# Optimization experiments

Measured on AMD Instinct MI355X. Metric: run time of the kernel, lower is better.

## Reference

```python
import jax, jax.numpy as jnp
import numpy as np

N_NODES = 100000
N_EDGES = 640000
NODE_DIM = 128
EDGE_DIM = 64
NUM_HEADS = 4
EPS = 1e-6


def setup_inputs() -> dict:
    key = jax.random.key(0)
    ks = jax.random.split(key, 12)
    s_attn = 1.0 / np.sqrt(NODE_DIM + EDGE_DIM)
    s_ev = 1.0 / np.sqrt(EDGE_DIM)
    s_out = 1.0 / np.sqrt(NODE_DIM)
    return {
        "node_features": jax.random.normal(ks[0], (N_NODES, NODE_DIM), jnp.float32),
        "edge_features": jax.random.normal(ks[1], (N_EDGES, EDGE_DIM), jnp.float32),
        "attn_W": jax.random.uniform(ks[2], (NODE_DIM + EDGE_DIM, NUM_HEADS), jnp.float32, -s_attn, s_attn),
        "attn_b": jax.random.uniform(ks[3], (NUM_HEADS,), jnp.float32, -s_attn, s_attn),
        "ev_W": jax.random.uniform(ks[4], (EDGE_DIM, NODE_DIM), jnp.float32, -s_ev, s_ev),
        "ev_b": jax.random.uniform(ks[5], (NODE_DIM,), jnp.float32, -s_ev, s_ev),
        "out1_W": jax.random.uniform(ks[6], (NODE_DIM, NODE_DIM), jnp.float32, -s_out, s_out),
        "out1_b": jax.random.uniform(ks[7], (NODE_DIM,), jnp.float32, -s_out, s_out),
        "out2_W": jax.random.uniform(ks[8], (NODE_DIM, NODE_DIM), jnp.float32, -s_out, s_out),
        "out2_b": jax.random.uniform(ks[9], (NODE_DIM,), jnp.float32, -s_out, s_out),
        "edge_index": jax.random.randint(ks[10], (2, N_EDGES), 0, N_NODES, jnp.int64 if jax.config.jax_enable_x64 else jnp.int32),
    }


def _segment_softmax_aggregate(values, scores_mean, dst, num_nodes):
    # segment max (empty segments -> -inf, then zeroed, matching torch include_self=False path)
    max_scores = jax.ops.segment_max(scores_mean, dst, num_segments=num_nodes)
    max_scores = jnp.where(jnp.isneginf(max_scores), jnp.zeros_like(max_scores), max_scores)
    exp_scores = jnp.exp(scores_mean - max_scores[dst])            # (E,)
    sum_exp = jax.ops.segment_sum(exp_scores, dst, num_segments=num_nodes)
    attn_weights = exp_scores / (sum_exp[dst] + EPS)               # (E,)
    # weighted scatter-add of edge values into destination nodes
    return jax.ops.segment_sum(values * attn_weights[:, None], dst, num_segments=num_nodes)


def reference(node_features, edge_features, attn_W, attn_b, ev_W, ev_b,
              out1_W, out1_b, out2_W, out2_b, edge_index):
    num_nodes = node_features.shape[0]
    dst = edge_index[1]
    h_dst = node_features[dst]                                     # (E, node_dim) gather
    attn_input = jnp.concatenate([h_dst, edge_features], axis=1)   # (E, node_dim+edge_dim)
    attn_scores = attn_input @ attn_W + attn_b                     # (E, H)
    scores_mean = attn_scores.mean(axis=1)                         # (E,)
    edge_values = edge_features @ ev_W + ev_b                      # (E, node_dim)
    messages = _segment_softmax_aggregate(edge_values, scores_mean, dst, num_nodes)
    update = jax.nn.relu(messages @ out1_W + out1_b) @ out2_W + out2_b
    return node_features + update
```

## Files before the change

### kernel.cpp

```cpp
#include <hip/hip_runtime.h>
#include <cstddef>

#define NN 100000
#define NE 640000
#define NB_SCAN 391
#define NTILE 1563

typedef short  short8   __attribute__((ext_vector_type(8)));
typedef float  f32x4    __attribute__((ext_vector_type(4)));
typedef ushort ushort4v __attribute__((ext_vector_type(4)));

__device__ __forceinline__ short f2bf(float f) {
    union { float f; unsigned u; } v; v.f = f;
    unsigned r = (v.u + 0x7fffu + ((v.u >> 16) & 1u)) >> 16;
    return (short)r;
}

__global__ __launch_bounds__(256) void k_pre(
    const float* __restrict__ W2, const int* __restrict__ dst_idx,
    int* __restrict__ count, ushort* __restrict__ W2t)
{
    const int gid = blockIdx.x * 256 + threadIdx.x;
    if (gid < 16384) {
        const int n = gid >> 7, k = gid & 127;
        W2t[gid] = (ushort)f2bf(W2[k * 128 + n]);
    }
    atomicAdd(&count[dst_idx[gid]], 1);
}

__global__ __launch_bounds__(128) void k_wfuse(
    const float* __restrict__ evW, const float* __restrict__ evb,
    const float* __restrict__ W1,
    ushort* __restrict__ EVW1t, float* __restrict__ EVB1)
{
    const int j = blockIdx.x;
    const int n = threadIdx.x;
    float acc = 0.f;
    #pragma unroll 8
    for (int c = 0; c < 128; ++c)
        acc = fmaf(evW[j * 128 + c], W1[c * 128 + n], acc);
    EVW1t[n * 64 + j] = (ushort)f2bf(acc);
    if (j == 0) {
        float ab = 0.f;
        #pragma unroll 8
        for (int c = 0; c < 128; ++c)
            ab = fmaf(evb[c], W1[c * 128 + n], ab);
        EVB1[n] = ab;
    }
}

__global__ __launch_bounds__(256) void k_scan_bsum(
    const int* __restrict__ count, int* __restrict__ bsum)
{
    __shared__ int s[256];
    const int t = threadIdx.x, i = blockIdx.x * 256 + t;
    s[t] = (i < NN) ? count[i] : 0;
    __syncthreads();
    for (int off = 128; off; off >>= 1) { if (t < off) s[t] += s[t + off]; __syncthreads(); }
    if (t == 0) bsum[blockIdx.x] = s[0];
}

__global__ __launch_bounds__(256) void k_scan_final(
    const int* __restrict__ count, const int* __restrict__ bsum,
    int* __restrict__ rowptr)
{
    __shared__ int s[256];
    __shared__ int red[4];
    const int t = threadIdx.x, i = blockIdx.x * 256 + t;
    const int v = (i < NN) ? count[i] : 0;
    s[t] = v;

    int part = 0;
    for (int b = t; b < blockIdx.x; b += 256) part += bsum[b];
    #pragma unroll
    for (int off = 32; off; off >>= 1) part += __shfl_xor(part, off);
    if ((t & 63) == 0) red[t >> 6] = part;
    __syncthreads();
    const int boff = red[0] + red[1] + red[2] + red[3];

    for (int off = 1; off < 256; off <<= 1) {
        const int x = (t >= off) ? s[t - off] : 0;
        __syncthreads();
        s[t] += x;
        __syncthreads();
    }
    if (i < NN) rowptr[i] = boff + s[t] - v;
    if (blockIdx.x == NB_SCAN - 1 && t == 255) rowptr[NN] = boff + s[255];
}

__global__ __launch_bounds__(256) void k_permute(
    const int* __restrict__ dst_idx, const int* __restrict__ rowptr,
    int* cursor, int* __restrict__ perm)
{
    const int e = blockIdx.x * 256 + threadIdx.x;
    const int dd = dst_idx[e];
    perm[rowptr[dd] + atomicAdd(&cursor[dd], 1)] = e;
}

__global__ __launch_bounds__(256) void k_agg_gather(
    const float* __restrict__ ef, const float* __restrict__ attn_W,
    const int* __restrict__ perm, const int* __restrict__ rowptr,
    ushort* __restrict__ agg, float* __restrict__ msum)
{
    const int t  = threadIdx.x;
    const int sl = t & 15;
    const int n  = blockIdx.x * 16 + (t >> 4);
    const int beg = rowptr[n], end = rowptr[n + 1];

    float4 wl;
    {
        const float4 r0 = *reinterpret_cast<const float4*>(attn_W + (128 + sl * 4 + 0) * 4);
        const float4 r1 = *reinterpret_cast<const float4*>(attn_W + (128 + sl * 4 + 1) * 4);
        const float4 r2 = *reinterpret_cast<const float4*>(attn_W + (128 + sl * 4 + 2) * 4);
        const float4 r3 = *reinterpret_cast<const float4*>(attn_W + (128 + sl * 4 + 3) * 4);
        wl.x = 0.25f * (r0.x + r0.y + r0.z + r0.w);
        wl.y = 0.25f * (r1.x + r1.y + r1.z + r1.w);
        wl.z = 0.25f * (r2.x + r2.y + r2.z + r2.w);
        wl.w = 0.25f * (r3.x + r3.y + r3.z + r3.w);
    }

    float m  = -3.0e38f;
    float se = 0.f;
    f32x4 acc = {0.f, 0.f, 0.f, 0.f};

    for (int i = beg; i < end; i += 8) {
        int pe[8];
        #pragma unroll
        for (int j = 0; j < 8; ++j)
            pe[j] = perm[(i + j < end) ? (i + j) : beg];
        float4 v[8];
        #pragma unroll
        for (int j = 0; j < 8; ++j)
            v[j] = *reinterpret_cast<const float4*>(ef + (size_t)pe[j] * 64 + sl * 4);
        float sc[8];
        #pragma unroll
        for (int j = 0; j < 8; ++j) {
            float x = v[j].x * wl.x + v[j].y * wl.y + v[j].z * wl.z + v[j].w * wl.w;
            #pragma unroll
            for (int off = 8; off; off >>= 1) x += __shfl_xor(x, off, 16);
            sc[j] = (i + j < end) ? x : -3.0e38f;
        }
        float bm = m;
        #pragma unroll
        for (int j = 0; j < 8; ++j) bm = fmaxf(bm, sc[j]);
        const float r = __expf(m - bm);
        acc[0] *= r; acc[1] *= r; acc[2] *= r; acc[3] *= r; se *= r;
        m = bm;
        #pragma unroll
        for (int j = 0; j < 8; ++j) {
            const float w = __expf(sc[j] - m);
            acc[0] = fmaf(w, v[j].x, acc[0]);
            acc[1] = fmaf(w, v[j].y, acc[1]);
            acc[2] = fmaf(w, v[j].z, acc[2]);
            acc[3] = fmaf(w, v[j].w, acc[3]);
            se += w;
        }
    }

    ushort4v o;
    o[0] = (ushort)f2bf(acc[0]); o[1] = (ushort)f2bf(acc[1]);
    o[2] = (ushort)f2bf(acc[2]); o[3] = (ushort)f2bf(acc[3]);
    *reinterpret_cast<ushort4v*>(agg + (size_t)n * 64 + sl * 4) = o;
    if (sl == 0) msum[n] = se;
}

__global__ __launch_bounds__(256, 3) void k_mega(
    const ushort* __restrict__ agg, const float* __restrict__ msum,
    const ushort* __restrict__ EVW1t, const float* __restrict__ EVB1,
    const float* __restrict__ b1, const ushort* __restrict__ W2t,
    const float* __restrict__ b2, const float* __restrict__ nf,
    ushort* __restrict__ h1w, float* __restrict__ out)
{
    __shared__ ushort wlds[128 * 128];
    __shared__ ushort tl[4][16][136];

    const int tid  = threadIdx.x;
    const int wid  = tid >> 6;
    const int lane = tid & 63;
    const int r    = lane & 15;
    const int g    = lane >> 4;
    const int prow = lane >> 2;
    const int pc   = lane & 3;

    for (int c = tid; c < 1024; c += 256) {
        const int n = c >> 3, k8 = c & 7;
        *reinterpret_cast<short8*>(&wlds[n * 64 + ((k8 ^ (n & 7)) * 8)]) =
            *reinterpret_cast<const short8*>(EVW1t + n * 64 + k8 * 8);
    }
    __syncthreads();

    float evb1c[8], b1c[8];
    #pragma unroll
    for (int nt = 0; nt < 8; ++nt) {
        evb1c[nt] = EVB1[nt * 16 + r];
        b1c[nt]   = b1[nt * 16 + r];
    }

    for (int bt = blockIdx.x; bt < NTILE; bt += gridDim.x) {
        const int n0 = bt * 64 + wid * 16;
        if (n0 >= NN) continue;
        const short8 aev0 = *reinterpret_cast<const short8*>(agg + (size_t)(n0 + r) * 64 + g * 8);
        const short8 aev1 = *reinterpret_cast<const short8*>(agg + (size_t)(n0 + r) * 64 + 32 + g * 8);
        float cf[4], cb[4];
        #pragma unroll
        for (int i = 0; i < 4; ++i) {
            const float s = msum[n0 + g * 4 + i];
            const float c = 1.f / (s + 1e-6f);
            cf[i] = c; cb[i] = s * c;
        }
        #pragma unroll
        for (int nt = 0; nt < 8; ++nt) {
            const int row = nt * 16 + r;
            const short8 w0 = *reinterpret_cast<const short8*>(
                &wlds[row * 64 + (((0 + g) ^ (r & 7)) * 8)]);
            const short8 w1 = *reinterpret_cast<const short8*>(
                &wlds[row * 64 + (((4 + g) ^ (r & 7)) * 8)]);
            f32x4 acc = {0.f, 0.f, 0.f, 0.f};
            acc = __builtin_amdgcn_mfma_f32_16x16x32_bf16(aev0, w0, acc, 0, 0, 0);
            acc = __builtin_amdgcn_mfma_f32_16x16x32_bf16(aev1, w1, acc, 0, 0, 0);
            #pragma unroll
            for (int i = 0; i < 4; ++i) {
                const float h = fmaxf(cf[i] * acc[i] + cb[i] * evb1c[nt] + b1c[nt], 0.f);
                tl[wid][g * 4 + i][nt * 16 + r] = (ushort)f2bf(h);
            }
        }
        asm volatile("s_waitcnt lgkmcnt(0)" ::: "memory");
        ushort* hrow = h1w + (size_t)(n0 + prow) * 128 + pc * 8;
        #pragma unroll
        for (int ch = 0; ch < 4; ++ch)
            *reinterpret_cast<short8*>(hrow + ch * 32) =
                *reinterpret_cast<const short8*>(&tl[wid][prow][pc * 8 + ch * 32]);
    }

    __syncthreads();
    for (int c = tid; c < 2048; c += 256) {
        const int n = c >> 4, k8 = c & 15;
        *reinterpret_cast<short8*>(&wlds[n * 128 + ((k8 ^ (n & 7)) * 8)]) =
            *reinterpret_cast<const short8*>(W2t + n * 128 + k8 * 8);
    }
    __syncthreads();

    float b2c[8];
    #pragma unroll
    for (int nt = 0; nt < 8; ++nt) b2c[nt] = b2[nt * 16 + r];

    for (int bt = blockIdx.x; bt < NTILE; bt += gridDim.x) {
        const int n0 = bt * 64 + wid * 16;
        if (n0 >= NN) continue;
        short8 a2[4];
        #pragma unroll
        for (int t = 0; t < 4; ++t)
            a2[t] = *reinterpret_cast<const short8*>(
                h1w + (size_t)(n0 + r) * 128 + t * 32 + g * 8);
        #pragma unroll
        for (int nt = 0; nt < 8; ++nt) {
            f32x4 acc = {0.f, 0.f, 0.f, 0.f};
            #pragma unroll
            for (int t = 0; t < 4; ++t) {
                const short8 w = *reinterpret_cast<const short8*>(
                    &wlds[(nt * 16 + r) * 128 + (((t * 4 + g) ^ (r & 7)) * 8)]);
                acc = __builtin_amdgcn_mfma_f32_16x16x32_bf16(a2[t], w, acc, 0, 0, 0);
            }
            #pragma unroll
            for (int i = 0; i < 4; ++i) {
                const size_t idx = (size_t)(n0 + g * 4 + i) * 128 + nt * 16 + r;
                out[idx] = nf[idx] + acc[i] + b2c[nt];
            }
        }
    }
}

extern "C" void kernel_launch(void* const* d_in, const int* in_sizes, int n_in,
                              void* d_out, int out_size, void* d_ws, size_t ws_size,
                              hipStream_t stream)
{
    const float* nf     = (const float*)d_in[0];
    const float* ef     = (const float*)d_in[1];
    const float* attn_W = (const float*)d_in[2];
    const float* evW    = (const float*)d_in[4];
    const float* evb    = (const float*)d_in[5];
    const float* W1     = (const float*)d_in[6];
    const float* b1     = (const float*)d_in[7];
    const float* W2     = (const float*)d_in[8];
    const float* b2     = (const float*)d_in[9];
    const int*   eidx   = (const int*)d_in[10];
    const int*   dst    = eidx + NE;
    float* out = (float*)d_out;

    char* ws = (char*)d_ws;
    int*    count  = (int*)   (ws + 0);
    int*    cursor = (int*)   (ws + 400000);
    int*    rowptr = (int*)   (ws + 800000);
    float*  msum   = (float*) (ws + 1200128);
    int*    perm   = (int*)   (ws + 1600128);
    ushort* agg    = (ushort*)(ws + 4160128);
    ushort* W2t    = (ushort*)(ws + 16960128);
    ushort* EVW1t  = (ushort*)(ws + 16992896);
    float*  EVB1   = (float*) (ws + 17009280);
    int*    bsum   = (int*)   (ws + 17009792);
    ushort* h1w    = (ushort*)(ws + 17011456);

    hipMemsetAsync(count, 0, 800000, stream);

    k_pre        <<<2500, 256, 0, stream>>>(W2, dst, count, W2t);
    k_wfuse      <<<64,   128, 0, stream>>>(evW, evb, W1, EVW1t, EVB1);
    k_scan_bsum  <<<NB_SCAN, 256, 0, stream>>>(count, bsum);
    k_scan_final <<<NB_SCAN, 256, 0, stream>>>(count, bsum, rowptr);
    k_permute    <<<2500, 256, 0, stream>>>(dst, rowptr, cursor, perm);
    k_agg_gather <<<6250, 256, 0, stream>>>(ef, attn_W, perm, rowptr, agg, msum);
    k_mega       <<<768,  256, 0, stream>>>(agg, msum, EVW1t, EVB1, b1, W2t, b2,
                                            nf, h1w, out);
}
```

Baseline: 157.8 us.

## Fuse both MLP layers per tile via LDS and replace memset with zero kernel

The two MLP phases in k_mega previously went through a global bf16 h1 buffer with a grid-wide second pass. Now both weight matrices stay resident in LDS, and each wave feeds its hidden tile straight from LDS into the second GEMM, so the h1 global write and read-back disappear. The larger LDS footprint drops occupancy to 2 blocks per CU and the grid to 512 blocks. The hipMemsetAsync is also replaced by a small zeroing kernel, likely to cut per-call API overhead.

New measurement: 145.1 us. -8.0%, faster.

```diff
diff --git a/kernel.cpp b/kernel.cpp
--- a/kernel.cpp
+++ b/kernel.cpp
@@ -14,6 +14,11 @@
     union { float f; unsigned u; } v; v.f = f;
     unsigned r = (v.u + 0x7fffu + ((v.u >> 16) & 1u)) >> 16;
     return (short)r;
+}
+
+__global__ __launch_bounds__(256) void k_zero(int4* __restrict__ p) {
+    const int i = blockIdx.x * 256 + threadIdx.x;
+    if (i < 50000) p[i] = make_int4(0, 0, 0, 0);
 }
 
 __global__ __launch_bounds__(256) void k_pre(
@@ -164,14 +169,15 @@
     if (sl == 0) msum[n] = se;
 }
 
-__global__ __launch_bounds__(256, 3) void k_mega(
+__global__ __launch_bounds__(256, 2) void k_mega(
     const ushort* __restrict__ agg, const float* __restrict__ msum,
     const ushort* __restrict__ EVW1t, const float* __restrict__ EVB1,
     const float* __restrict__ b1, const ushort* __restrict__ W2t,
     const float* __restrict__ b2, const float* __restrict__ nf,
-    ushort* __restrict__ h1w, float* __restrict__ out)
-{
-    __shared__ ushort wlds[128 * 128];
+    float* __restrict__ out)
+{
+    __shared__ ushort wev[128 * 64];
+    __shared__ ushort ww2[128 * 128];
     __shared__ ushort tl[4][16][136];
 
     const int tid  = threadIdx.x;
@@ -179,26 +185,31 @@
     const int lane = tid & 63;
     const int r    = lane & 15;
     const int g    = lane >> 4;
-    const int prow = lane >> 2;
-    const int pc   = lane & 3;
 
     for (int c = tid; c < 1024; c += 256) {
         const int n = c >> 3, k8 = c & 7;
-        *reinterpret_cast<short8*>(&wlds[n * 64 + ((k8 ^ (n & 7)) * 8)]) =
+        *reinterpret_cast<short8*>(&wev[n * 64 + ((k8 ^ (n & 7)) * 8)]) =
             *reinterpret_cast<const short8*>(EVW1t + n * 64 + k8 * 8);
     }
+    for (int c = tid; c < 2048; c += 256) {
+        const int n = c >> 4, k8 = c & 15;
+        *reinterpret_cast<short8*>(&ww2[n * 128 + ((k8 ^ (n & 7)) * 8)]) =
+            *reinterpret_cast<const short8*>(W2t + n * 128 + k8 * 8);
+    }
     __syncthreads();
 
-    float evb1c[8], b1c[8];
+    float evb1c[8], b1c[8], b2c[8];
     #pragma unroll
     for (int nt = 0; nt < 8; ++nt) {
         evb1c[nt] = EVB1[nt * 16 + r];
         b1c[nt]   = b1[nt * 16 + r];
+        b2c[nt]   = b2[nt * 16 + r];
     }
 
     for (int bt = blockIdx.x; bt < NTILE; bt += gridDim.x) {
         const int n0 = bt * 64 + wid * 16;
         if (n0 >= NN) continue;
+
         const short8 aev0 = *reinterpret_cast<const short8*>(agg + (size_t)(n0 + r) * 64 + g * 8);
         const short8 aev1 = *reinterpret_cast<const short8*>(agg + (size_t)(n0 + r) * 64 + 32 + g * 8);
         float cf[4], cb[4];
@@ -208,13 +219,14 @@
             const float c = 1.f / (s + 1e-6f);
             cf[i] = c; cb[i] = s * c;
         }
+
         #pragma unroll
         for (int nt = 0; nt < 8; ++nt) {
             const int row = nt * 16 + r;
             const short8 w0 = *reinterpret_cast<const short8*>(
-                &wlds[row * 64 + (((0 + g) ^ (r & 7)) * 8)]);
+                &wev[row * 64 + (((0 + g) ^ (r & 7)) * 8)]);
             const short8 w1 = *reinterpret_cast<const short8*>(
-                &wlds[row * 64 + (((4 + g) ^ (r & 7)) * 8)]);
+                &wev[row * 64 + (((4 + g) ^ (r & 7)) * 8)]);
             f32x4 acc = {0.f, 0.f, 0.f, 0.f};
             acc = __builtin_amdgcn_mfma_f32_16x16x32_bf16(aev0, w0, acc, 0, 0, 0);
             acc = __builtin_amdgcn_mfma_f32_16x16x32_bf16(aev1, w1, acc, 0, 0, 0);
@@ -225,40 +237,20 @@
             }
         }
         asm volatile("s_waitcnt lgkmcnt(0)" ::: "memory");
-        ushort* hrow = h1w + (size_t)(n0 + prow) * 128 + pc * 8;
-        #pragma unroll
-        for (int ch = 0; ch < 4; ++ch)
-            *reinterpret_cast<short8*>(hrow + ch * 32) =
-                *reinterpret_cast<const short8*>(&tl[wid][prow][pc * 8 + ch * 32]);
-    }
-
-    __syncthreads();
-    for (int c = tid; c < 2048; c += 256) {
-        const int n = c >> 4, k8 = c & 15;
-        *reinterpret_cast<short8*>(&wlds[n * 128 + ((k8 ^ (n & 7)) * 8)]) =
-            *reinterpret_cast<const short8*>(W2t + n * 128 + k8 * 8);
-    }
-    __syncthreads();
-
-    float b2c[8];
-    #pragma unroll
-    for (int nt = 0; nt < 8; ++nt) b2c[nt] = b2[nt * 16 + r];
-
-    for (int bt = blockIdx.x; bt < NTILE; bt += gridDim.x) {
-        const int n0 = bt * 64 + wid * 16;
-        if (n0 >= NN) continue;
+
         short8 a2[4];
         #pragma unroll
         for (int t = 0; t < 4; ++t)
-            a2[t] = *reinterpret_cast<const short8*>(
-                h1w + (size_t)(n0 + r) * 128 + t * 32 + g * 8);
+            a2[t] = *reinterpret_cast<const short8*>(&tl[wid][r][t * 32 + g * 8]);
+        asm volatile("s_waitcnt lgkmcnt(0)" ::: "memory");
+
         #pragma unroll
         for (int nt = 0; nt < 8; ++nt) {
             f32x4 acc = {0.f, 0.f, 0.f, 0.f};
             #pragma unroll
             for (int t = 0; t < 4; ++t) {
                 const short8 w = *reinterpret_cast<const short8*>(
-                    &wlds[(nt * 16 + r) * 128 + (((t * 4 + g) ^ (r & 7)) * 8)]);
+                    &ww2[(nt * 16 + r) * 128 + (((t * 4 + g) ^ (r & 7)) * 8)]);
                 acc = __builtin_amdgcn_mfma_f32_16x16x32_bf16(a2[t], w, acc, 0, 0, 0);
             }
             #pragma unroll
@@ -298,16 +290,13 @@
     ushort* EVW1t  = (ushort*)(ws + 16992896);
     float*  EVB1   = (float*) (ws + 17009280);
     int*    bsum   = (int*)   (ws + 17009792);
-    ushort* h1w    = (ushort*)(ws + 17011456);
-
-    hipMemsetAsync(count, 0, 800000, stream);
-
+
+    k_zero       <<<196,  256, 0, stream>>>((int4*)count);
     k_pre        <<<2500, 256, 0, stream>>>(W2, dst, count, W2t);
     k_wfuse      <<<64,   128, 0, stream>>>(evW, evb, W1, EVW1t, EVB1);
     k_scan_bsum  <<<NB_SCAN, 256, 0, stream>>>(count, bsum);
     k_scan_final <<<NB_SCAN, 256, 0, stream>>>(count, bsum, rowptr);
     k_permute    <<<2500, 256, 0, stream>>>(dst, rowptr, cursor, perm);
     k_agg_gather <<<6250, 256, 0, stream>>>(ef, attn_W, perm, rowptr, agg, msum);
-    k_mega       <<<768,  256, 0, stream>>>(agg, msum, EVW1t, EVB1, b1, W2t, b2,
-                                            nf, h1w, out);
-}
+    k_mega       <<<512,  256, 0, stream>>>(agg, msum, EVW1t, EVB1, b1, W2t, b2, nf, out);
+}
```
